# Optimization experiments

Measured on AMD Instinct MI355X. Metric: run time of the kernel, lower is better.

## Reference

```python
import jax, jax.numpy as jnp
import numpy as np

CHEB_K = 3

def setup_inputs() -> dict:
    key = jax.random.key(0)
    ks = jax.random.split(key, 6)
    bs, node, in_dim, out_dim = 8, 1024, 64, 64
    d_e, t_d, embed_dim = 10, 6, 16
    return {
        "x": jax.random.normal(ks[0], (bs, node, in_dim), dtype=jnp.float32),
        "node_emb": jax.random.normal(ks[1], (node, d_e), dtype=jnp.float32),
        "t": jax.random.normal(ks[2], (bs, t_d), dtype=jnp.float32),
        "n_t": jax.random.normal(ks[3], (bs, t_d), dtype=jnp.float32),
        "p": jnp.zeros((1,), dtype=jnp.float32),
        "weights_pool": jax.random.normal(ks[4], (embed_dim, CHEB_K, in_dim, out_dim), dtype=jnp.float32),
        "bias_pool": jax.random.normal(ks[5], (embed_dim, out_dim), dtype=jnp.float32),
    }

def reference(x, node_emb, t, n_t, p, weights_pool, bias_pool):
    # x: [bs, node, in_dim]; node_emb: [node, d_e]; t, n_t: [bs, t_d]
    bs, node, _ = x.shape
    # static adjacency logits shared across batch: [node, node]
    a = node_emb @ node_emb.T
    # temporal scalar per batch: bmm of [bs,1,t_d] x [bs,t_d,1] -> [bs,1,1]
    a_t = jnp.einsum('bd,bd->b', n_t, t)[:, None, None]
    _a = a[None, :, :] + a_t                       # [bs, node, node]
    # period=False branch
    A = jax.nn.softmax(jax.nn.relu(_a), axis=2)    # [bs, node, node]
    # Chebyshev recursion: T0=I, T1=A, Tk = 2A@T_{k-1} - T_{k-2}
    I = jnp.broadcast_to(jnp.eye(node, dtype=x.dtype), (bs, node, node))
    supports = [I, A]
    for _ in range(2, CHEB_K):
        supports.append(jnp.matmul(2.0 * A, supports[-1]) - supports[-2])
    cheb = jnp.stack(supports, axis=1)             # [bs, k, node, node]
    # node+time embedding: [bs, node, d_e + t_d] = [bs, node, embed_dim]
    emb = jnp.concatenate(
        [jnp.broadcast_to(node_emb[None], (bs, node, node_emb.shape[1])),
         jnp.broadcast_to(n_t[:, None, :], (bs, node, n_t.shape[1]))], axis=-1)
    # graph conv: x_g[b,n,k,i] = sum_m cheb[b,k,n,m] x[b,m,i]
    x_g = jnp.einsum('bknm,bmc->bnkc', cheb, x)
    # fuse per-node weight generation into final contraction (same math as
    # weights = einsum('bnd,dkio->bnkio') followed by einsum('bnki,bnkio->bno'))
    out = jnp.einsum('bnki,bnd,dkio->bno', x_g, emb, weights_pool)
    bias = jnp.einsum('bnd,do->bno', emb, bias_pool)
    return out + bias
```

## Files before the change

kernel.cpp:

```cpp
#include <hip/hip_runtime.h>
#include <hip/hip_bf16.h>

#define NODE 1024
#define BS 8
#define XG_K 208

struct alignas(8) bf4 { __hip_bfloat16 a, b, c, d; };
typedef short short8 __attribute__((ext_vector_type(8)));
typedef float f32x16 __attribute__((ext_vector_type(16)));

__global__ __launch_bounds__(256) void k_attn(const float* __restrict__ ne,
                                              const float* __restrict__ t,
                                              const float* __restrict__ nt,
                                              __hip_bfloat16* __restrict__ A16) {
    __shared__ float nel[NODE * 11];
    __shared__ float redm[8][4], reds[8][4];
    int n = blockIdx.x, tid = threadIdx.x;
    int lane = tid & 63, wid = tid >> 6;

    for (int i = tid; i < NODE * 10; i += 256) nel[(i / 10) * 11 + (i % 10)] = ne[i];

    float at[8];
#pragma unroll
    for (int b = 0; b < 8; ++b) {
        float s = 0.f;
#pragma unroll
        for (int j = 0; j < 6; ++j) s += nt[b * 6 + j] * t[b * 6 + j];
        at[b] = s;
    }
    __syncthreads();

    float nr[10];
#pragma unroll
    for (int d = 0; d < 10; ++d) nr[d] = nel[n * 11 + d];

    float v[4];
#pragma unroll
    for (int c = 0; c < 4; ++c) {
        int m = tid + c * 256;
        float s = 0.f;
#pragma unroll
        for (int d = 0; d < 10; ++d) s += nr[d] * nel[m * 11 + d];
        v[c] = s;
    }

#pragma unroll
    for (int b = 0; b < 8; ++b) {
        float u[4], mx = 0.f;
#pragma unroll
        for (int c = 0; c < 4; ++c) { u[c] = fmaxf(v[c] + at[b], 0.f); mx = fmaxf(mx, u[c]); }
#pragma unroll
        for (int off = 32; off > 0; off >>= 1) mx = fmaxf(mx, __shfl_xor(mx, off));
        if (lane == 0) redm[b][wid] = mx;
        __syncthreads();
        mx = fmaxf(fmaxf(redm[b][0], redm[b][1]), fmaxf(redm[b][2], redm[b][3]));

        float s = 0.f;
#pragma unroll
        for (int c = 0; c < 4; ++c) { u[c] = __expf(u[c] - mx); s += u[c]; }
#pragma unroll
        for (int off = 32; off > 0; off >>= 1) s += __shfl_xor(s, off);
        if (lane == 0) reds[b][wid] = s;
        __syncthreads();
        s = reds[b][0] + reds[b][1] + reds[b][2] + reds[b][3];
        float inv = 1.f / s;

        __hip_bfloat16* dst = A16 + (((size_t)(b << 10) + n) << 10);
#pragma unroll
        for (int c = 0; c < 4; ++c) dst[tid + c * 256] = __float2bfloat16(u[c] * inv);
    }
}

__global__ void k_prep(const float* __restrict__ x, __hip_bfloat16* __restrict__ xT,
                       __hip_bfloat16* __restrict__ xg) {
    int b = blockIdx.x >> 4;
    int n0 = (blockIdx.x & 15) * 64;
    __shared__ __hip_bfloat16 T[64][72];
    int tid = threadIdx.x;
    int nloc = tid >> 2, f0 = (tid & 3) * 16;
    size_t row = (size_t)(b << 10) + n0 + nloc;
    {
        const float* src = x + row * 64 + f0;
        __hip_bfloat16* dst = xg + row * XG_K + f0;
#pragma unroll
        for (int j = 0; j < 16; j += 4) {
            float4 vv = *(const float4*)(src + j);
            bf4 o;
            o.a = __float2bfloat16(vv.x); o.b = __float2bfloat16(vv.y);
            o.c = __float2bfloat16(vv.z); o.d = __float2bfloat16(vv.w);
            *(bf4*)(dst + j) = o;
            T[f0 + j][nloc] = o.a; T[f0 + j + 1][nloc] = o.b;
            T[f0 + j + 2][nloc] = o.c; T[f0 + j + 3][nloc] = o.d;
        }
    }
    if (tid < 64) {
        __hip_bfloat16* d2 = xg + ((size_t)(b << 10) + n0 + tid) * XG_K + 192;
        d2[0] = __float2bfloat16(1.0f);
#pragma unroll
        for (int j = 1; j < 16; ++j) d2[j] = __float2bfloat16(0.0f);
    }
    __syncthreads();
    {
        int f = tid >> 2, c0 = (tid & 3) * 16;
        __hip_bfloat16* dst = xT + ((size_t)b * 64 + f) * 1024 + n0 + c0;
#pragma unroll
        for (int j = 0; j < 16; ++j) dst[j] = T[f][c0 + j];
    }
}

__global__ void k_wprep(const float* __restrict__ W, const float* __restrict__ bp,
                        __hip_bfloat16* __restrict__ wt) {
    int d = blockIdx.x;
    __shared__ __hip_bfloat16 T[64 * XG_K];
    int tid = threadIdx.x;
    const float* Wd = W + (size_t)d * 192 * 64;
    for (int i = tid; i < 192 * 64; i += 256) {
        int k = i >> 6, o = i & 63;
        T[o * XG_K + k] = __float2bfloat16(Wd[i]);
    }
    if (tid < 64) {
        T[tid * XG_K + 192] = __float2bfloat16(bp[d * 64 + tid]);
#pragma unroll
        for (int j = 1; j < 16; ++j) T[tid * XG_K + 192 + j] = __float2bfloat16(0.0f);
    }
    __syncthreads();
    __hip_bfloat16* dst = wt + (size_t)d * 64 * XG_K;
    for (int i = tid; i < 64 * XG_K; i += 256) dst[i] = T[i];
}

template<bool FIRST>
__global__ void k_spmm_mfma(const __hip_bfloat16* __restrict__ A16,
                            const __hip_bfloat16* __restrict__ srcT,
                            const float* __restrict__ xres,
                            __hip_bfloat16* __restrict__ xg,
                            __hip_bfloat16* __restrict__ youtT) {
    int b = blockIdx.x >> 5;
    int n0 = (blockIdx.x & 31) * 32;
    int tid = threadIdx.x;
    int fh = tid >> 6;
    int lane = tid & 63;
    int l31 = lane & 31, hi = lane >> 5;

    const __hip_bfloat16* pa = srcT + ((size_t)b * 64 + fh * 32 + l31) * 1024 + hi * 8;
    const __hip_bfloat16* pb = A16 + ((size_t)b << 20) + (size_t)(n0 + l31) * 1024 + hi * 8;

    f32x16 acc0, acc1;
#pragma unroll
    for (int i = 0; i < 16; ++i) { acc0[i] = 0.f; acc1[i] = 0.f; }

    short8 ac[4], bc[4];
#pragma unroll
    for (int j = 0; j < 4; ++j) {
        ac[j] = *(const short8*)(pa + j * 16);
        bc[j] = *(const short8*)(pb + j * 16);
    }
    for (int g = 1; g < 16; ++g) {
        short8 an[4], bn[4];
#pragma unroll
        for (int j = 0; j < 4; ++j) {
            an[j] = *(const short8*)(pa + g * 64 + j * 16);
            bn[j] = *(const short8*)(pb + g * 64 + j * 16);
        }
        acc0 = __builtin_amdgcn_mfma_f32_32x32x16_bf16(ac[0], bc[0], acc0, 0, 0, 0);
        acc1 = __builtin_amdgcn_mfma_f32_32x32x16_bf16(ac[1], bc[1], acc1, 0, 0, 0);
        acc0 = __builtin_amdgcn_mfma_f32_32x32x16_bf16(ac[2], bc[2], acc0, 0, 0, 0);
        acc1 = __builtin_amdgcn_mfma_f32_32x32x16_bf16(ac[3], bc[3], acc1, 0, 0, 0);
#pragma unroll
        for (int j = 0; j < 4; ++j) { ac[j] = an[j]; bc[j] = bn[j]; }
    }
    acc0 = __builtin_amdgcn_mfma_f32_32x32x16_bf16(ac[0], bc[0], acc0, 0, 0, 0);
    acc1 = __builtin_amdgcn_mfma_f32_32x32x16_bf16(ac[1], bc[1], acc1, 0, 0, 0);
    acc0 = __builtin_amdgcn_mfma_f32_32x32x16_bf16(ac[2], bc[2], acc0, 0, 0, 0);
    acc1 = __builtin_amdgcn_mfma_f32_32x32x16_bf16(ac[3], bc[3], acc1, 0, 0, 0);

#pragma unroll
    for (int i = 0; i < 16; ++i) acc0[i] += acc1[i];

    int node = n0 + l31;
    size_t row = (size_t)(b << 10) + node;
    const int base = FIRST ? 64 : 128;
#pragma unroll
    for (int rg = 0; rg < 4; ++rg) {
        int fb = fh * 32 + hi * 4 + rg * 8;
        float vx = acc0[rg * 4], vy = acc0[rg * 4 + 1];
        float vz = acc0[rg * 4 + 2], vw = acc0[rg * 4 + 3];
        if (!FIRST) {
            float4 xv = *(const float4*)(xres + row * 64 + fb);
            vx = 2.f * vx - xv.x; vy = 2.f * vy - xv.y;
            vz = 2.f * vz - xv.z; vw = 2.f * vw - xv.w;
        }
        bf4 o;
        o.a = __float2bfloat16(vx); o.b = __float2bfloat16(vy);
        o.c = __float2bfloat16(vz); o.d = __float2bfloat16(vw);
        *(bf4*)(xg + row * XG_K + base + fb) = o;
    }
    if (FIRST) {
#pragma unroll
        for (int r = 0; r < 16; ++r) {
            int f = fh * 32 + hi * 4 + (r >> 2) * 8 + (r & 3);
            youtT[((size_t)b * 64 + f) * 1024 + node] = __float2bfloat16(acc0[r]);
        }
    }
}

__global__ __launch_bounds__(512) void k_fuse(const __hip_bfloat16* __restrict__ xg,
                                              const __hip_bfloat16* __restrict__ wt,
                                              const float* __restrict__ ne,
                                              const float* __restrict__ nt,
                                              float* __restrict__ out) {
    __shared__ float P[8][32][66];
    int m0 = blockIdx.x * 32;
    int tid = threadIdx.x;
    int w = tid >> 6;
    int lane = tid & 63;
    int l31 = lane & 31, hi = lane >> 5;
    int b = m0 >> 10;
    int n = (m0 & 1023) + l31;

    int d0 = 2 * w, d1 = 2 * w + 1;
    float e0 = (d0 < 10) ? ne[n * 10 + d0] : nt[b * 6 + (d0 - 10)];
    float e1 = (d1 < 10) ? ne[n * 10 + d1] : nt[b * 6 + (d1 - 10)];

    short8 xf[13];
    const __hip_bfloat16* px = xg + (size_t)(m0 + l31) * XG_K + hi * 8;
#pragma unroll
    for (int k = 0; k < 13; ++k) xf[k] = *(const short8*)(px + k * 16);

    f32x16 z00, z01, z10, z11;
#pragma unroll
    for (int i = 0; i < 16; ++i) { z00[i] = 0.f; z01[i] = 0.f; z10[i] = 0.f; z11[i] = 0.f; }

    const __hip_bfloat16* pw0 = wt + ((size_t)d0 * 64 + l31) * XG_K + hi * 8;
    const __hip_bfloat16* pw1 = pw0 + (size_t)64 * XG_K;
#pragma unroll
    for (int k = 0; k < 13; ++k) {
        short8 a00 = *(const short8*)(pw0 + k * 16);
        short8 a01 = *(const short8*)(pw0 + (size_t)32 * XG_K + k * 16);
        short8 a10 = *(const short8*)(pw1 + k * 16);
        short8 a11 = *(const short8*)(pw1 + (size_t)32 * XG_K + k * 16);
        z00 = __builtin_amdgcn_mfma_f32_32x32x16_bf16(a00, xf[k], z00, 0, 0, 0);
        z01 = __builtin_amdgcn_mfma_f32_32x32x16_bf16(a01, xf[k], z01, 0, 0, 0);
        z10 = __builtin_amdgcn_mfma_f32_32x32x16_bf16(a10, xf[k], z10, 0, 0, 0);
        z11 = __builtin_amdgcn_mfma_f32_32x32x16_bf16(a11, xf[k], z11, 0, 0, 0);
    }

#pragma unroll
    for (int r = 0; r < 16; ++r) {
        int o = (r & 3) + 8 * (r >> 2) + 4 * hi;
        P[w][l31][o]      = e0 * z00[r] + e1 * z10[r];
        P[w][l31][o + 32] = e0 * z01[r] + e1 * z11[r];
    }
    __syncthreads();

    int m = tid >> 4, o0 = (tid & 15) * 4;
    float s0 = 0.f, s1 = 0.f, s2 = 0.f, s3 = 0.f;
#pragma unroll
    for (int ww = 0; ww < 8; ++ww) {
        s0 += P[ww][m][o0];
        s1 += P[ww][m][o0 + 1];
        s2 += P[ww][m][o0 + 2];
        s3 += P[ww][m][o0 + 3];
    }
    *(float4*)(out + (size_t)(m0 + m) * 64 + o0) = make_float4(s0, s1, s2, s3);
}

extern "C" void kernel_launch(void* const* d_in, const int* in_sizes, int n_in,
                              void* d_out, int out_size, void* d_ws, size_t ws_size,
                              hipStream_t stream) {
    const float* x  = (const float*)d_in[0];
    const float* ne = (const float*)d_in[1];
    const float* t  = (const float*)d_in[2];
    const float* nt = (const float*)d_in[3];
    const float* W  = (const float*)d_in[5];
    const float* bp = (const float*)d_in[6];
    float* out = (float*)d_out;

    __hip_bfloat16* wsb = (__hip_bfloat16*)d_ws;
    __hip_bfloat16* A16 = wsb;
    __hip_bfloat16* xT  = wsb + 8388608;
    __hip_bfloat16* y1T = wsb + 8912896;
    __hip_bfloat16* xg  = wsb + 9437184;
    __hip_bfloat16* wt  = wsb + 11141120;

    k_attn<<<NODE, 256, 0, stream>>>(ne, t, nt, A16);
    k_prep<<<BS * 16, 256, 0, stream>>>(x, xT, xg);
    k_wprep<<<16, 256, 0, stream>>>(W, bp, wt);
    k_spmm_mfma<true ><<<BS * 32, 128, 0, stream>>>(A16, xT,  x, xg, y1T);
    k_spmm_mfma<false><<<BS * 32, 128, 0, stream>>>(A16, y1T, x, xg, nullptr);
    k_fuse<<<BS * (NODE / 32), 512, 0, stream>>>(xg, wt, ne, nt, out);
}
```

Baseline: 131.3 us.

## Restructure attention rows per wave, merge prep kernels, split-K spmm across waves

```diff
diff --git a/kernel.cpp b/kernel.cpp
--- a/kernel.cpp
+++ b/kernel.cpp
@@ -14,9 +14,9 @@
                                               const float* __restrict__ nt,
                                               __hip_bfloat16* __restrict__ A16) {
     __shared__ float nel[NODE * 11];
-    __shared__ float redm[8][4], reds[8][4];
-    int n = blockIdx.x, tid = threadIdx.x;
-    int lane = tid & 63, wid = tid >> 6;
+    int tid = threadIdx.x;
+    int w = tid >> 6, lane = tid & 63;
+    int n = (blockIdx.x << 2) + w;
 
     for (int i = tid; i < NODE * 10; i += 256) nel[(i / 10) * 11 + (i % 10)] = ne[i];
 
@@ -34,171 +34,178 @@
 #pragma unroll
     for (int d = 0; d < 10; ++d) nr[d] = nel[n * 11 + d];
 
-    float v[4];
-#pragma unroll
-    for (int c = 0; c < 4; ++c) {
-        int m = tid + c * 256;
+    float v[16];
+#pragma unroll
+    for (int j = 0; j < 16; ++j) {
+        const float* row = &nel[(lane + (j << 6)) * 11];
         float s = 0.f;
 #pragma unroll
-        for (int d = 0; d < 10; ++d) s += nr[d] * nel[m * 11 + d];
-        v[c] = s;
+        for (int d = 0; d < 10; ++d) s += nr[d] * row[d];
+        v[j] = s;
     }
 
 #pragma unroll
     for (int b = 0; b < 8; ++b) {
-        float u[4], mx = 0.f;
-#pragma unroll
-        for (int c = 0; c < 4; ++c) { u[c] = fmaxf(v[c] + at[b], 0.f); mx = fmaxf(mx, u[c]); }
-#pragma unroll
-        for (int off = 32; off > 0; off >>= 1) mx = fmaxf(mx, __shfl_xor(mx, off));
-        if (lane == 0) redm[b][wid] = mx;
+        float u[16], s = 0.f;
+#pragma unroll
+        for (int j = 0; j < 16; ++j) {
+            u[j] = __expf(fmaxf(v[j] + at[b], 0.f));
+            s += u[j];
+        }
+#pragma unroll
+        for (int off = 32; off > 0; off >>= 1) s += __shfl_xor(s, off);
+        float inv = 1.f / s;
+        __hip_bfloat16* dst = A16 + (((size_t)(b << 10) + n) << 10);
+#pragma unroll
+        for (int j = 0; j < 16; ++j) dst[lane + (j << 6)] = __float2bfloat16(u[j] * inv);
+    }
+}
+
+__global__ __launch_bounds__(256) void k_prepw(const float* __restrict__ x,
+                                               const float* __restrict__ W,
+                                               const float* __restrict__ bp,
+                                               __hip_bfloat16* __restrict__ xT,
+                                               __hip_bfloat16* __restrict__ xg,
+                                               __hip_bfloat16* __restrict__ wt) {
+    __shared__ __hip_bfloat16 sh[64 * XG_K];
+    int tid = threadIdx.x;
+
+    if (blockIdx.x < 128) {
+        typedef __hip_bfloat16 row72[72];
+        row72* T = (row72*)sh;
+        int b = blockIdx.x >> 4;
+        int n0 = (blockIdx.x & 15) * 64;
+        int nloc = tid >> 2, f0 = (tid & 3) * 16;
+        size_t row = (size_t)(b << 10) + n0 + nloc;
+        {
+            const float* src = x + row * 64 + f0;
+            __hip_bfloat16* dst = xg + row * XG_K + f0;
+#pragma unroll
+            for (int j = 0; j < 16; j += 4) {
+                float4 vv = *(const float4*)(src + j);
+                bf4 o;
+                o.a = __float2bfloat16(vv.x); o.b = __float2bfloat16(vv.y);
+                o.c = __float2bfloat16(vv.z); o.d = __float2bfloat16(vv.w);
+                *(bf4*)(dst + j) = o;
+                T[f0 + j][nloc] = o.a; T[f0 + j + 1][nloc] = o.b;
+                T[f0 + j + 2][nloc] = o.c; T[f0 + j + 3][nloc] = o.d;
+            }
+        }
+        if (tid < 64) {
+            __hip_bfloat16* d2 = xg + ((size_t)(b << 10) + n0 + tid) * XG_K + 192;
+            d2[0] = __float2bfloat16(1.0f);
+#pragma unroll
+            for (int j = 1; j < 16; ++j) d2[j] = __float2bfloat16(0.0f);
+        }
         __syncthreads();
-        mx = fmaxf(fmaxf(redm[b][0], redm[b][1]), fmaxf(redm[b][2], redm[b][3]));
-
-        float s = 0.f;
-#pragma unroll
-        for (int c = 0; c < 4; ++c) { u[c] = __expf(u[c] - mx); s += u[c]; }
-#pragma unroll
-        for (int off = 32; off > 0; off >>= 1) s += __shfl_xor(s, off);
-        if (lane == 0) reds[b][wid] = s;
+        {
+            int f = tid >> 2, c0 = (tid & 3) * 16;
+            __hip_bfloat16* dst = xT + ((size_t)b * 64 + f) * 1024 + n0 + c0;
+#pragma unroll
+            for (int j = 0; j < 16; ++j) dst[j] = T[f][c0 + j];
+        }
+    } else {
+        int d = blockIdx.x - 128;
+        const float* Wd = W + (size_t)d * 192 * 64;
+        for (int i = tid; i < 192 * 64; i += 256) {
+            int k = i >> 6, o = i & 63;
+            sh[o * XG_K + k] = __float2bfloat16(Wd[i]);
+        }
+        if (tid < 64) {
+            sh[tid * XG_K + 192] = __float2bfloat16(bp[d * 64 + tid]);
+#pragma unroll
+            for (int j = 1; j < 16; ++j) sh[tid * XG_K + 192 + j] = __float2bfloat16(0.0f);
+        }
         __syncthreads();
-        s = reds[b][0] + reds[b][1] + reds[b][2] + reds[b][3];
-        float inv = 1.f / s;
-
-        __hip_bfloat16* dst = A16 + (((size_t)(b << 10) + n) << 10);
-#pragma unroll
-        for (int c = 0; c < 4; ++c) dst[tid + c * 256] = __float2bfloat16(u[c] * inv);
-    }
-}
-
-__global__ void k_prep(const float* __restrict__ x, __hip_bfloat16* __restrict__ xT,
-                       __hip_bfloat16* __restrict__ xg) {
-    int b = blockIdx.x >> 4;
-    int n0 = (blockIdx.x & 15) * 64;
-    __shared__ __hip_bfloat16 T[64][72];
-    int tid = threadIdx.x;
-    int nloc = tid >> 2, f0 = (tid & 3) * 16;
-    size_t row = (size_t)(b << 10) + n0 + nloc;
-    {
-        const float* src = x + row * 64 + f0;
-        __hip_bfloat16* dst = xg + row * XG_K + f0;
-#pragma unroll
-        for (int j = 0; j < 16; j += 4) {
-            float4 vv = *(const float4*)(src + j);
+        __hip_bfloat16* dst = wt + (size_t)d * 64 * XG_K;
+        for (int i = tid; i < 64 * XG_K; i += 256) dst[i] = sh[i];
+    }
+}
+
+#define LOADG(slot, g) do {                                                   \
+    const __hip_bfloat16* qa = pa + (g) * 64;                                 \
+    const __hip_bfloat16* qb = pb + (g) * 64;                                 \
+    as[slot][0] = *(const short8*)(qa);      as[slot][1] = *(const short8*)(qa + 16); \
+    as[slot][2] = *(const short8*)(qa + 32); as[slot][3] = *(const short8*)(qa + 48); \
+    bs[slot][0] = *(const short8*)(qb);      bs[slot][1] = *(const short8*)(qb + 16); \
+    bs[slot][2] = *(const short8*)(qb + 32); bs[slot][3] = *(const short8*)(qb + 48); \
+} while (0)
+
+template<bool FIRST>
+__global__ __launch_bounds__(256) void k_spmm_mfma(const __hip_bfloat16* __restrict__ A16,
+                                                   const __hip_bfloat16* __restrict__ srcT,
+                                                   const float* __restrict__ xres,
+                                                   __hip_bfloat16* __restrict__ xg,
+                                                   __hip_bfloat16* __restrict__ youtT) {
+    __shared__ float P[2][32][67];
+    int b = blockIdx.x >> 5;
+    int n0 = (blockIdx.x & 31) << 5;
+    int tid = threadIdx.x;
+    int wv = tid >> 6, lane = tid & 63;
+    int fh = wv & 1, kh = wv >> 1;
+    int l31 = lane & 31, hi = lane >> 5;
+
+    const __hip_bfloat16* pa = srcT + ((size_t)b * 64 + fh * 32 + l31) * 1024 + (kh << 9) + hi * 8;
+    const __hip_bfloat16* pb = A16 + ((size_t)b << 20) + (size_t)(n0 + l31) * 1024 + (kh << 9) + hi * 8;
+
+    f32x16 acc0, acc1;
+#pragma unroll
+    for (int i = 0; i < 16; ++i) { acc0[i] = 0.f; acc1[i] = 0.f; }
+
+    short8 as[3][4], bs[3][4];
+    LOADG(0, 0);
+    LOADG(1, 1);
+#pragma unroll
+    for (int g = 0; g < 8; ++g) {
+        if (g + 2 < 8) { LOADG((g + 2) % 3, g + 2); }
+        int cu = g % 3;
+        acc0 = __builtin_amdgcn_mfma_f32_32x32x16_bf16(as[cu][0], bs[cu][0], acc0, 0, 0, 0);
+        acc1 = __builtin_amdgcn_mfma_f32_32x32x16_bf16(as[cu][1], bs[cu][1], acc1, 0, 0, 0);
+        acc0 = __builtin_amdgcn_mfma_f32_32x32x16_bf16(as[cu][2], bs[cu][2], acc0, 0, 0, 0);
+        acc1 = __builtin_amdgcn_mfma_f32_32x32x16_bf16(as[cu][3], bs[cu][3], acc1, 0, 0, 0);
+    }
+#pragma unroll
+    for (int i = 0; i < 16; ++i) acc0[i] += acc1[i];
+
+    if (kh == 1) {
+#pragma unroll
+        for (int r = 0; r < 16; ++r) {
+            int f = hi * 4 + (r >> 2) * 8 + (r & 3);
+            P[fh][l31][f] = acc0[r];
+        }
+    }
+    __syncthreads();
+    if (kh == 0) {
+#pragma unroll
+        for (int r = 0; r < 16; ++r) {
+            int f = hi * 4 + (r >> 2) * 8 + (r & 3);
+            acc0[r] += P[fh][l31][f];
+        }
+
+        int node = n0 + l31;
+        size_t row = (size_t)(b << 10) + node;
+        const int base = FIRST ? 64 : 128;
+#pragma unroll
+        for (int rg = 0; rg < 4; ++rg) {
+            int fb = fh * 32 + hi * 4 + rg * 8;
+            float vx = acc0[rg * 4], vy = acc0[rg * 4 + 1];
+            float vz = acc0[rg * 4 + 2], vw = acc0[rg * 4 + 3];
+            if (!FIRST) {
+                float4 xv = *(const float4*)(xres + row * 64 + fb);
+                vx = 2.f * vx - xv.x; vy = 2.f * vy - xv.y;
+                vz = 2.f * vz - xv.z; vw = 2.f * vw - xv.w;
+            }
             bf4 o;
-            o.a = __float2bfloat16(vv.x); o.b = __float2bfloat16(vv.y);
-            o.c = __float2bfloat16(vv.z); o.d = __float2bfloat16(vv.w);
-            *(bf4*)(dst + j) = o;
-            T[f0 + j][nloc] = o.a; T[f0 + j + 1][nloc] = o.b;
-            T[f0 + j + 2][nloc] = o.c; T[f0 + j + 3][nloc] = o.d;
-        }
-    }
-    if (tid < 64) {
-        __hip_bfloat16* d2 = xg + ((size_t)(b << 10) + n0 + tid) * XG_K + 192;
-        d2[0] = __float2bfloat16(1.0f);
-#pragma unroll
-        for (int j = 1; j < 16; ++j) d2[j] = __float2bfloat16(0.0f);
-    }
-    __syncthreads();
-    {
-        int f = tid >> 2, c0 = (tid & 3) * 16;
-        __hip_bfloat16* dst = xT + ((size_t)b * 64 + f) * 1024 + n0 + c0;
-#pragma unroll
-        for (int j = 0; j < 16; ++j) dst[j] = T[f][c0 + j];
-    }
-}
-
-__global__ void k_wprep(const float* __restrict__ W, const float* __restrict__ bp,
-                        __hip_bfloat16* __restrict__ wt) {
-    int d = blockIdx.x;
-    __shared__ __hip_bfloat16 T[64 * XG_K];
-    int tid = threadIdx.x;
-    const float* Wd = W + (size_t)d * 192 * 64;
-    for (int i = tid; i < 192 * 64; i += 256) {
-        int k = i >> 6, o = i & 63;
-        T[o * XG_K + k] = __float2bfloat16(Wd[i]);
-    }
-    if (tid < 64) {
-        T[tid * XG_K + 192] = __float2bfloat16(bp[d * 64 + tid]);
-#pragma unroll
-        for (int j = 1; j < 16; ++j) T[tid * XG_K + 192 + j] = __float2bfloat16(0.0f);
-    }
-    __syncthreads();
-    __hip_bfloat16* dst = wt + (size_t)d * 64 * XG_K;
-    for (int i = tid; i < 64 * XG_K; i += 256) dst[i] = T[i];
-}
-
-template<bool FIRST>
-__global__ void k_spmm_mfma(const __hip_bfloat16* __restrict__ A16,
-                            const __hip_bfloat16* __restrict__ srcT,
-                            const float* __restrict__ xres,
-                            __hip_bfloat16* __restrict__ xg,
-                            __hip_bfloat16* __restrict__ youtT) {
-    int b = blockIdx.x >> 5;
-    int n0 = (blockIdx.x & 31) * 32;
-    int tid = threadIdx.x;
-    int fh = tid >> 6;
-    int lane = tid & 63;
-    int l31 = lane & 31, hi = lane >> 5;
-
-    const __hip_bfloat16* pa = srcT + ((size_t)b * 64 + fh * 32 + l31) * 1024 + hi * 8;
-    const __hip_bfloat16* pb = A16 + ((size_t)b << 20) + (size_t)(n0 + l31) * 1024 + hi * 8;
-
-    f32x16 acc0, acc1;
-#pragma unroll
-    for (int i = 0; i < 16; ++i) { acc0[i] = 0.f; acc1[i] = 0.f; }
-
-    short8 ac[4], bc[4];
-#pragma unroll
-    for (int j = 0; j < 4; ++j) {
-        ac[j] = *(const short8*)(pa + j * 16);
-        bc[j] = *(const short8*)(pb + j * 16);
-    }
-    for (int g = 1; g < 16; ++g) {
-        short8 an[4], bn[4];
-#pragma unroll
-        for (int j = 0; j < 4; ++j) {
-            an[j] = *(const short8*)(pa + g * 64 + j * 16);
-            bn[j] = *(const short8*)(pb + g * 64 + j * 16);
-        }
-        acc0 = __builtin_amdgcn_mfma_f32_32x32x16_bf16(ac[0], bc[0], acc0, 0, 0, 0);
-        acc1 = __builtin_amdgcn_mfma_f32_32x32x16_bf16(ac[1], bc[1], acc1, 0, 0, 0);
-        acc0 = __builtin_amdgcn_mfma_f32_32x32x16_bf16(ac[2], bc[2], acc0, 0, 0, 0);
-        acc1 = __builtin_amdgcn_mfma_f32_32x32x16_bf16(ac[3], bc[3], acc1, 0, 0, 0);
-#pragma unroll
-        for (int j = 0; j < 4; ++j) { ac[j] = an[j]; bc[j] = bn[j]; }
-    }
-    acc0 = __builtin_amdgcn_mfma_f32_32x32x16_bf16(ac[0], bc[0], acc0, 0, 0, 0);
-    acc1 = __builtin_amdgcn_mfma_f32_32x32x16_bf16(ac[1], bc[1], acc1, 0, 0, 0);
-    acc0 = __builtin_amdgcn_mfma_f32_32x32x16_bf16(ac[2], bc[2], acc0, 0, 0, 0);
-    acc1 = __builtin_amdgcn_mfma_f32_32x32x16_bf16(ac[3], bc[3], acc1, 0, 0, 0);
-
-#pragma unroll
-    for (int i = 0; i < 16; ++i) acc0[i] += acc1[i];
-
-    int node = n0 + l31;
-    size_t row = (size_t)(b << 10) + node;
-    const int base = FIRST ? 64 : 128;
-#pragma unroll
-    for (int rg = 0; rg < 4; ++rg) {
-        int fb = fh * 32 + hi * 4 + rg * 8;
-        float vx = acc0[rg * 4], vy = acc0[rg * 4 + 1];
-        float vz = acc0[rg * 4 + 2], vw = acc0[rg * 4 + 3];
-        if (!FIRST) {
-            float4 xv = *(const float4*)(xres + row * 64 + fb);
-            vx = 2.f * vx - xv.x; vy = 2.f * vy - xv.y;
-            vz = 2.f * vz - xv.z; vw = 2.f * vw - xv.w;
-        }
-        bf4 o;
-        o.a = __float2bfloat16(vx); o.b = __float2bfloat16(vy);
-        o.c = __float2bfloat16(vz); o.d = __float2bfloat16(vw);
-        *(bf4*)(xg + row * XG_K + base + fb) = o;
-    }
-    if (FIRST) {
-#pragma unroll
-        for (int r = 0; r < 16; ++r) {
-            int f = fh * 32 + hi * 4 + (r >> 2) * 8 + (r & 3);
-            youtT[((size_t)b * 64 + f) * 1024 + node] = __float2bfloat16(acc0[r]);
+            o.a = __float2bfloat16(vx); o.b = __float2bfloat16(vy);
+            o.c = __float2bfloat16(vz); o.d = __float2bfloat16(vw);
+            *(bf4*)(xg + row * XG_K + base + fb) = o;
+        }
+        if (FIRST) {
+#pragma unroll
+            for (int r = 0; r < 16; ++r) {
+                int f = fh * 32 + hi * 4 + (r >> 2) * 8 + (r & 3);
+                youtT[((size_t)b * 64 + f) * 1024 + node] = __float2bfloat16(acc0[r]);
+            }
         }
     }
 }
@@ -208,7 +215,7 @@
                                               const float* __restrict__ ne,
                                               const float* __restrict__ nt,
                                               float* __restrict__ out) {
-    __shared__ float P[8][32][66];
+    __shared__ float P[8][32][67];
     int m0 = blockIdx.x * 32;
     int tid = threadIdx.x;
     int w = tid >> 6;
@@ -282,10 +289,9 @@
     __hip_bfloat16* xg  = wsb + 9437184;
     __hip_bfloat16* wt  = wsb + 11141120;
 
-    k_attn<<<NODE, 256, 0, stream>>>(ne, t, nt, A16);
-    k_prep<<<BS * 16, 256, 0, stream>>>(x, xT, xg);
-    k_wprep<<<16, 256, 0, stream>>>(W, bp, wt);
-    k_spmm_mfma<true ><<<BS * 32, 128, 0, stream>>>(A16, xT,  x, xg, y1T);
-    k_spmm_mfma<false><<<BS * 32, 128, 0, stream>>>(A16, y1T, x, xg, nullptr);
+    k_attn<<<NODE / 4, 256, 0, stream>>>(ne, t, nt, A16);
+    k_prepw<<<144, 256, 0, stream>>>(x, W, bp, xT, xg, wt);
+    k_spmm_mfma<true ><<<BS * 32, 256, 0, stream>>>(A16, xT,  x, xg, y1T);
+    k_spmm_mfma<false><<<BS * 32, 256, 0, stream>>>(A16, y1T, x, xg, nullptr);
     k_fuse<<<BS * (NODE / 32), 512, 0, stream>>>(xg, wt, ne, nt, out);
 }
```

Result: faster. 117.2 us (-10.7%).
